# Performance work log

Measured on AMD Instinct MI355X. Metric: run time of the kernel, lower is better.

The kernel has to match this reference:

```python
import jax, jax.numpy as jnp
import numpy as np

N_MESH, N_GRID, N_EDGE = 2562, 16384, 49152
D, EDGE_DIM, OUT_DIM = 512, 4, 128
LN_EPS = 1e-5


def _mlp_ln(x, w1, b1, w2, b2, g, beta):
    # Linear -> ReLU -> Linear -> LayerNorm (activate_final=False, use_layer_norm=True)
    h = jax.nn.relu(x @ w1 + b1)
    h = h @ w2 + b2
    mu = jnp.mean(h, axis=-1, keepdims=True)
    var = jnp.var(h, axis=-1, keepdims=True)
    return (h - mu) * jax.lax.rsqrt(var + LN_EPS) * g + beta


def setup_inputs() -> dict:
    key = jax.random.key(0)
    ks = iter(jax.random.split(key, 40))

    def W(i, o):
        return (jax.random.normal(next(ks), (i, o), jnp.float32) / np.float32(np.sqrt(i)))

    inp = {
        "input_mesh_nodes": jax.random.normal(next(ks), (N_MESH, D), jnp.float32),
        "input_grid_nodes": jax.random.normal(next(ks), (N_GRID, D), jnp.float32),
        "input_edge_attr": jax.random.normal(next(ks), (N_EDGE, EDGE_DIM), jnp.float32),
        "edge_index": jnp.stack([
            jax.random.randint(next(ks), (N_EDGE,), 0, N_MESH, jnp.int32),  # senders (mesh)
            jax.random.randint(next(ks), (N_EDGE,), 0, N_GRID, jnp.int32),  # receivers (grid)
        ], axis=0),
        # edges_mlp: EDGE_DIM -> D -> D, LN
        "emlp_w1": W(EDGE_DIM, D), "emlp_b1": jnp.zeros((D,), jnp.float32),
        "emlp_w2": W(D, D), "emlp_b2": jnp.zeros((D,), jnp.float32),
        "emlp_g": jnp.ones((D,), jnp.float32), "emlp_beta": jnp.zeros((D,), jnp.float32),
        # gnn message MLP: 3D -> D -> D, LN   (cat(x_i, x_j, edge_attr))
        "ge_w1": W(3 * D, D), "ge_b1": jnp.zeros((D,), jnp.float32),
        "ge_w2": W(D, D), "ge_b2": jnp.zeros((D,), jnp.float32),
        "ge_g": jnp.ones((D,), jnp.float32), "ge_beta": jnp.zeros((D,), jnp.float32),
        # gnn node MLP: 2D -> D -> D, LN   (cat(receiver_x, aggr))
        "gn_w1": W(2 * D, D), "gn_b1": jnp.zeros((D,), jnp.float32),
        "gn_w2": W(D, D), "gn_b2": jnp.zeros((D,), jnp.float32),
        "gn_g": jnp.ones((D,), jnp.float32), "gn_beta": jnp.zeros((D,), jnp.float32),
        # grid_mlp_final: D -> D -> OUT_DIM, LN
        "fin_w1": W(D, D), "fin_b1": jnp.zeros((D,), jnp.float32),
        "fin_w2": W(D, OUT_DIM), "fin_b2": jnp.zeros((OUT_DIM,), jnp.float32),
        "fin_g": jnp.ones((OUT_DIM,), jnp.float32), "fin_beta": jnp.zeros((OUT_DIM,), jnp.float32),
    }
    return inp


def reference(input_mesh_nodes, input_grid_nodes, input_edge_attr, edge_index,
              emlp_w1, emlp_b1, emlp_w2, emlp_b2, emlp_g, emlp_beta,
              ge_w1, ge_b1, ge_w2, ge_b2, ge_g, ge_beta,
              gn_w1, gn_b1, gn_w2, gn_b2, gn_g, gn_beta,
              fin_w1, fin_b1, fin_w2, fin_b2, fin_g, fin_beta):
    # edge embedding MLP
    edges_emb = _mlp_ln(input_edge_attr, emlp_w1, emlp_b1, emlp_w2, emlp_b2, emlp_g, emlp_beta)
    senders, receivers = edge_index[0], edge_index[1]
    x_i = input_grid_nodes[receivers]   # receiver (grid) features gathered per edge
    x_j = input_mesh_nodes[senders]     # sender (mesh) features gathered per edge
    # per-edge message MLP on cat(x_i, x_j, edge_attr)
    msg = _mlp_ln(jnp.concatenate([x_i, x_j, edges_emb], axis=-1),
                  ge_w1, ge_b1, ge_w2, ge_b2, ge_g, ge_beta)  # [E, D]
    # scatter-add messages to receiver grid nodes (aggr='add')
    aggr = jax.ops.segment_sum(msg, receivers, num_segments=N_GRID)  # [N_GRID, D]
    # node update MLP on cat(receiver_x, aggr)
    gnn_out = _mlp_ln(jnp.concatenate([input_grid_nodes, aggr], axis=-1),
                      gn_w1, gn_b1, gn_w2, gn_b2, gn_g, gn_beta)
    latent_grid_nodes = input_grid_nodes + gnn_out  # residual
    return _mlp_ln(latent_grid_nodes, fin_w1, fin_b1, fin_w2, fin_b2, fin_g, fin_beta)
```

## Files before the change

kernel.cpp:

```cpp
#include <hip/hip_runtime.h>
#include <hip/hip_bf16.h>
#include <stdint.h>

#define LN_EPS 1e-5f

typedef __hip_bfloat16 bf16;
typedef short short8 __attribute__((ext_vector_type(8)));
typedef float f32x4 __attribute__((ext_vector_type(4)));

static __device__ __forceinline__ float bf2f(short s) {
    unsigned int u = ((unsigned int)(unsigned short)s) << 16;
    return __uint_as_float(u);
}
static __device__ __forceinline__ short f2bf(float x) {
    __hip_bfloat16 h = __float2bfloat16(x);
    return *reinterpret_cast<short*>(&h);
}

static __device__ __forceinline__ void gload16(const void* g, void* l) {
    __builtin_amdgcn_global_load_lds((const __attribute__((address_space(1))) void*)g,
                                     (__attribute__((address_space(3))) void*)l, 16, 0, 0);
}

struct TDesc { const float* src; bf16* dst; int K; int N; int kOff; };
struct TDescs { TDesc d[9]; };

__global__ void transpose_all_kernel(TDescs descs) {
    TDesc t = descs.d[blockIdx.z];
    int kb = blockIdx.x * 32, nb = blockIdx.y * 32;
    if (kb >= t.K || nb >= t.N) return;
    __shared__ float tile[32][33];
    int tx = threadIdx.x & 31, ty = threadIdx.x >> 5;
    for (int i = ty; i < 32; i += 8) {
        int k = kb + i, n = nb + tx;
        tile[i][tx] = (k < t.K && n < t.N) ? t.src[(size_t)(t.kOff + k) * t.N + n] : 0.f;
    }
    __syncthreads();
    for (int i = ty; i < 32; i += 8) {
        int n = nb + i, k = kb + tx;
        if (n < t.N && k < t.K)
            t.dst[(size_t)n * t.K + k] = __float2bfloat16(tile[tx][i]);
    }
}

__global__ void cvt_bf16_kernel(const float* __restrict__ src, bf16* __restrict__ dst, int n) {
    int i = blockIdx.x * 256 + threadIdx.x;
    int idx = i * 4;
    if (idx >= n) return;
    float4 v = *(const float4*)(src + idx);
    dst[idx + 0] = __float2bfloat16(v.x);
    dst[idx + 1] = __float2bfloat16(v.y);
    dst[idx + 2] = __float2bfloat16(v.z);
    dst[idx + 3] = __float2bfloat16(v.w);
}

__global__ void edge_l1_kernel(const float* __restrict__ attr, const float* __restrict__ w1,
                               const float* __restrict__ b1, bf16* __restrict__ h1, int E) {
    int e = blockIdx.x * 4 + (threadIdx.x >> 6);
    if (e >= E) return;
    int lane = threadIdx.x & 63;
    int d0 = lane * 8;
    float4 a = *(const float4*)(attr + (size_t)e * 4);
    float av[4] = {a.x, a.y, a.z, a.w};
    float s[8];
    {
        float4 c0 = *(const float4*)(b1 + d0), c1 = *(const float4*)(b1 + d0 + 4);
        s[0]=c0.x; s[1]=c0.y; s[2]=c0.z; s[3]=c0.w; s[4]=c1.x; s[5]=c1.y; s[6]=c1.z; s[7]=c1.w;
    }
#pragma unroll
    for (int k = 0; k < 4; k++) {
        float4 w0 = *(const float4*)(w1 + k * 512 + d0);
        float4 w1v = *(const float4*)(w1 + k * 512 + d0 + 4);
        float wv[8] = {w0.x, w0.y, w0.z, w0.w, w1v.x, w1v.y, w1v.z, w1v.w};
#pragma unroll
        for (int j = 0; j < 8; j++) s[j] += av[k] * wv[j];
    }
    short8 o;
#pragma unroll
    for (int j = 0; j < 8; j++) o[j] = f2bf(fmaxf(s[j], 0.f));
    *(short8*)(h1 + (size_t)e * 512 + d0) = o;
}

template <int EPI>
__global__ __launch_bounds__(256, 2) void gemm_bt_kernel(
    const bf16* __restrict__ A, const bf16* __restrict__ BT,
    const float* __restrict__ bias, bf16* __restrict__ C, int M, int N, int K,
    const bf16* __restrict__ gridp, const bf16* __restrict__ meshp,
    const int* __restrict__ send, const int* __restrict__ recv) {
    __shared__ short SMEM[2 * 2 * 128 * 64];
    const int t = threadIdx.x;
    const int lane = t & 63, w = t >> 6;
    const int wm = w >> 1, wn = w & 1;
    const int lr = lane & 15, lh = lane >> 4;

    int gx = gridDim.x, gy = gridDim.y;
    int orig = blockIdx.y * gx + blockIdx.x;
    int bx, by;
    if ((gy & 7) == 0) {
        int xcd = orig & 7, t2 = orig >> 3;
        bx = t2 % gx;
        by = xcd + 8 * (t2 / gx);
    } else { bx = blockIdx.x; by = blockIdx.y; }
    const int row0 = by * 128;
    const int col0 = bx * 128;

    const int sr3 = lane >> 3;
    const int su = (lane & 7) ^ sr3;
    const int srow = w * 32 + sr3;
    const int scol = su * 8;
    const bf16* gaP[4];
    const bf16* gbP[4];
#pragma unroll
    for (int i = 0; i < 4; i++) {
        int ra = row0 + srow + i * 8; if (ra >= M) ra = M - 1;
        int rb = col0 + srow + i * 8; if (rb >= N) rb = N - 1;
        gaP[i] = A + (size_t)ra * K + scol;
        gbP[i] = BT + (size_t)rb * K + scol;
    }

    auto STAGE = [&](int b, int k0) {
        short* la = SMEM + b * 16384 + w * 32 * 64;
        short* lb = la + 8192;
#pragma unroll
        for (int i = 0; i < 4; i++) {
            gload16(gaP[i] + k0, la + i * 8 * 64);
            gload16(gbP[i] + k0, lb + i * 8 * 64);
        }
    };

    f32x4 acc[4][4];
#pragma unroll
    for (int i = 0; i < 4; i++)
#pragma unroll
        for (int j = 0; j < 4; j++) acc[i][j] = {0.f, 0.f, 0.f, 0.f};

    const int T = K >> 6;
    STAGE(0, 0);
    __syncthreads();

    int cur = 0;
    for (int tt = 0; tt < T; ++tt) {
        if (tt + 1 < T) STAGE(cur ^ 1, (tt + 1) << 6);
        const short* Ac = SMEM + cur * 16384;
        const short* Bc = Ac + 8192;
#pragma unroll
        for (int kk = 0; kk < 64; kk += 32) {
            short8 af[4], bfv[4];
#pragma unroll
            for (int mf = 0; mf < 4; mf++) {
                int rowa = wm * 64 + mf * 16 + lr;
                int ua = ((kk >> 3) + lh) ^ (rowa & 7);
                af[mf] = *(const short8*)&Ac[rowa * 64 + ua * 8];
            }
#pragma unroll
            for (int nf = 0; nf < 4; nf++) {
                int rowb = wn * 64 + nf * 16 + lr;
                int ub = ((kk >> 3) + lh) ^ (rowb & 7);
                bfv[nf] = *(const short8*)&Bc[rowb * 64 + ub * 8];
            }
#pragma unroll
            for (int mf = 0; mf < 4; mf++)
#pragma unroll
                for (int nf = 0; nf < 4; nf++)
                    acc[mf][nf] = __builtin_amdgcn_mfma_f32_16x16x32_bf16(
                        af[mf], bfv[nf], acc[mf][nf], 0, 0, 0);
        }
        __syncthreads();
        cur ^= 1;
    }

    short* Cw = SMEM + w * (32 * 66);
    const int rgrp = lane >> 3, u = lane & 7;
#pragma unroll
    for (int hp = 0; hp < 2; hp++) {
#pragma unroll
        for (int mf2 = 0; mf2 < 2; mf2++) {
            int mf = hp * 2 + mf2;
#pragma unroll
            for (int nf = 0; nf < 4; nf++)
#pragma unroll
                for (int r2 = 0; r2 < 4; r2++) {
                    int rl = mf2 * 16 + lh * 4 + r2;
                    Cw[rl * 66 + nf * 16 + lr] = f2bf(acc[mf][nf][r2]);
                }
        }
#pragma unroll
        for (int rr = 0; rr < 4; rr++) {
            int rl = rr * 8 + rgrp;
            int grow = row0 + wm * 64 + hp * 32 + rl;
            int gcol = col0 + wn * 64 + u * 8;
            short8 vv = *(const short8*)&Cw[rl * 66 + u * 8];
            float vf[8];
#pragma unroll
            for (int j = 0; j < 8; j++) vf[j] = bf2f(vv[j]);
            if (EPI >= 1) {
                float4 c0 = *(const float4*)(bias + gcol);
                float4 c1 = *(const float4*)(bias + gcol + 4);
                float bb[8] = {c0.x, c0.y, c0.z, c0.w, c1.x, c1.y, c1.z, c1.w};
#pragma unroll
                for (int j = 0; j < 8; j++) vf[j] += bb[j];
            }
            if (EPI == 3) {
                int e = grow < M ? grow : M - 1;
                int rn = recv[e], sn = send[e];
                short8 gp = *(const short8*)(gridp + (size_t)rn * 512 + gcol);
                short8 mp = *(const short8*)(meshp + (size_t)sn * 512 + gcol);
#pragma unroll
                for (int j = 0; j < 8; j++) vf[j] += bf2f(gp[j]) + bf2f(mp[j]);
            }
            if (EPI >= 2) {
#pragma unroll
                for (int j = 0; j < 8; j++) vf[j] = fmaxf(vf[j], 0.f);
            }
            short8 o;
#pragma unroll
            for (int j = 0; j < 8; j++) o[j] = f2bf(vf[j]);
            if (grow < M && gcol < N)
                *(short8*)(C + (size_t)grow * N + gcol) = o;
        }
    }
}

template <int MODE, int DN>
__global__ void ln_kernel(const bf16* __restrict__ X, const float* __restrict__ gw,
                          const float* __restrict__ bw, bf16* __restrict__ outb,
                          float* __restrict__ outf, const bf16* __restrict__ resid, int R) {
    constexpr int EPL = DN / 64;
    int row = blockIdx.x * 4 + (threadIdx.x >> 6);
    if (row >= R) return;
    int lane = threadIdx.x & 63;
    const bf16* xr = X + (size_t)row * DN + lane * EPL;
    float v[EPL];
    if constexpr (EPL == 8) {
        short8 t8 = *(const short8*)xr;
#pragma unroll
        for (int j = 0; j < 8; j++) v[j] = bf2f(t8[j]);
    } else {
#pragma unroll
        for (int j = 0; j < EPL; j++) v[j] = __bfloat162float(xr[j]);
    }
    float s = 0.f, s2 = 0.f;
#pragma unroll
    for (int j = 0; j < EPL; j++) { s += v[j]; s2 += v[j] * v[j]; }
#pragma unroll
    for (int o = 32; o > 0; o >>= 1) {
        s += __shfl_xor(s, o, 64);
        s2 += __shfl_xor(s2, o, 64);
    }
    float mu = s * (1.f / DN);
    float var = s2 * (1.f / DN) - mu * mu;
    float rs = rsqrtf(var + LN_EPS);
    int d0 = lane * EPL;

    if constexpr (MODE == 0) {
        short8 o;
#pragma unroll
        for (int j = 0; j < EPL; j++)
            o[j] = f2bf((v[j] - mu) * rs * gw[d0 + j] + bw[d0 + j]);
        *(short8*)(outb + (size_t)row * DN + d0) = o;
    } else if constexpr (MODE == 2) {
        short8 rv = *(const short8*)(resid + (size_t)row * DN + d0);
        short8 o;
#pragma unroll
        for (int j = 0; j < EPL; j++) {
            float y = (v[j] - mu) * rs * gw[d0 + j] + bw[d0 + j];
            o[j] = f2bf(bf2f(rv[j]) + y);
        }
        *(short8*)(outb + (size_t)row * DN + d0) = o;
    } else {
#pragma unroll
        for (int j = 0; j < EPL; j++)
            outf[(size_t)row * DN + d0 + j] = (v[j] - mu) * rs * gw[d0 + j] + bw[d0 + j];
    }
}

__global__ void ln_stats_kernel(const bf16* __restrict__ X, float2* __restrict__ stats, int R) {
    int row = blockIdx.x * 4 + (threadIdx.x >> 6);
    if (row >= R) return;
    int lane = threadIdx.x & 63;
    short8 t8 = *(const short8*)(X + (size_t)row * 512 + lane * 8);
    float s = 0.f, s2 = 0.f;
#pragma unroll
    for (int j = 0; j < 8; j++) {
        float x = bf2f(t8[j]);
        s += x; s2 += x * x;
    }
#pragma unroll
    for (int o = 32; o > 0; o >>= 1) {
        s += __shfl_xor(s, o, 64);
        s2 += __shfl_xor(s2, o, 64);
    }
    float mu = s * (1.f / 512.f);
    float var = s2 * (1.f / 512.f) - mu * mu;
    if (lane == 0) stats[row] = make_float2(mu, rsqrtf(var + LN_EPS));
}

__global__ void degree_kernel(const int* __restrict__ recv, int* __restrict__ deg, int E) {
    int e = blockIdx.x * 256 + threadIdx.x;
    if (e < E) atomicAdd(&deg[recv[e]], 1);
}

__global__ void scan_kernel(const int* __restrict__ deg, int* __restrict__ off) {
    __shared__ int partial[1024];
    int t = threadIdx.x;
    int base = t * 16;
    int v[16];
    int s = 0;
#pragma unroll
    for (int i = 0; i < 16; i++) { v[i] = deg[base + i]; s += v[i]; }
    partial[t] = s;
    __syncthreads();
    for (int o = 1; o < 1024; o <<= 1) {
        int x = (t >= o) ? partial[t - o] : 0;
        __syncthreads();
        partial[t] += x;
        __syncthreads();
    }
    int run = (t == 0) ? 0 : partial[t - 1];
#pragma unroll
    for (int i = 0; i < 16; i++) { off[base + i] = run; run += v[i]; }
    if (t == 1023) off[16384] = run;
}

__global__ void scatter_kernel(const int* __restrict__ recv, const int* __restrict__ off,
                               int* __restrict__ cnt, int* __restrict__ edges, int E) {
    int e = blockIdx.x * 256 + threadIdx.x;
    if (e < E) {
        int r = recv[e];
        int p = atomicAdd(&cnt[r], 1);
        edges[off[r] + p] = e;
    }
}

__global__ void aggregate_kernel(const bf16* __restrict__ T5, const float2* __restrict__ stats,
                                 const float* __restrict__ gw, const float* __restrict__ bw,
                                 const bf16* __restrict__ gridb,
                                 const int* __restrict__ off, const int* __restrict__ edges,
                                 bf16* __restrict__ X2, int G) {
    int g = blockIdx.x * 4 + (threadIdx.x >> 6);
    if (g >= G) return;
    int lane = threadIdx.x & 63;
    int d0 = lane * 8;
    float gg[8], bb[8];
    {
        float4 a = *(const float4*)(gw + d0), b = *(const float4*)(gw + d0 + 4);
        gg[0]=a.x; gg[1]=a.y; gg[2]=a.z; gg[3]=a.w; gg[4]=b.x; gg[5]=b.y; gg[6]=b.z; gg[7]=b.w;
        float4 c = *(const float4*)(bw + d0), d = *(const float4*)(bw + d0 + 4);
        bb[0]=c.x; bb[1]=c.y; bb[2]=c.z; bb[3]=c.w; bb[4]=d.x; bb[5]=d.y; bb[6]=d.z; bb[7]=d.w;
    }
    float s[8] = {0.f, 0.f, 0.f, 0.f, 0.f, 0.f, 0.f, 0.f};
    int a = off[g], b = off[g + 1];
    for (int i = a; i < b; i++) {
        int e = edges[i];
        float2 st = stats[e];
        short8 m = *(const short8*)(T5 + (size_t)e * 512 + d0);
#pragma unroll
        for (int j = 0; j < 8; j++)
            s[j] += (bf2f(m[j]) - st.x) * st.y * gg[j] + bb[j];
    }
    *(short8*)(X2 + (size_t)g * 1024 + d0) = *(const short8*)(gridb + (size_t)g * 512 + d0);
    short8 o;
#pragma unroll
    for (int j = 0; j < 8; j++) o[j] = f2bf(s[j]);
    *(short8*)(X2 + (size_t)g * 1024 + 512 + d0) = o;
}

extern "C" void kernel_launch(void* const* d_in, const int* in_sizes, int n_in,
                              void* d_out, int out_size, void* d_ws, size_t ws_size,
                              hipStream_t stream) {
    const int NM = 2562, NG = 16384, NE = 49152;
    const float* mesh   = (const float*)d_in[0];
    const float* grid   = (const float*)d_in[1];
    const float* attr   = (const float*)d_in[2];
    const int*   eidx   = (const int*)d_in[3];
    const int*   send   = eidx;
    const int*   recv   = eidx + NE;
    const float* emlp_w1 = (const float*)d_in[4];
    const float* emlp_b1 = (const float*)d_in[5];
    const float* emlp_w2 = (const float*)d_in[6];
    const float* emlp_b2 = (const float*)d_in[7];
    const float* emlp_g  = (const float*)d_in[8];
    const float* emlp_be = (const float*)d_in[9];
    const float* ge_w1 = (const float*)d_in[10];
    const float* ge_b1 = (const float*)d_in[11];
    const float* ge_w2 = (const float*)d_in[12];
    const float* ge_b2 = (const float*)d_in[13];
    const float* ge_g  = (const float*)d_in[14];
    const float* ge_be = (const float*)d_in[15];
    const float* gn_w1 = (const float*)d_in[16];
    const float* gn_b1 = (const float*)d_in[17];
    const float* gn_w2 = (const float*)d_in[18];
    const float* gn_b2 = (const float*)d_in[19];
    const float* gn_g  = (const float*)d_in[20];
    const float* gn_be = (const float*)d_in[21];
    const float* fin_w1 = (const float*)d_in[22];
    const float* fin_b1 = (const float*)d_in[23];
    const float* fin_w2 = (const float*)d_in[24];
    const float* fin_b2 = (const float*)d_in[25];
    const float* fin_g  = (const float*)d_in[26];
    const float* fin_be = (const float*)d_in[27];

    char* p = (char*)d_ws;
    auto take = [&](size_t bytes) -> char* {
        char* r = p;
        p += (bytes + 255) & ~(size_t)255;
        return r;
    };
    bf16* emlp_w2T = (bf16*)take((size_t)512 * 512 * 2);
    bf16* geA_T    = (bf16*)take((size_t)512 * 512 * 2);
    bf16* geB_T    = (bf16*)take((size_t)512 * 512 * 2);
    bf16* geC_T    = (bf16*)take((size_t)512 * 512 * 2);
    bf16* ge_w2T   = (bf16*)take((size_t)512 * 512 * 2);
    bf16* gn_w1T   = (bf16*)take((size_t)512 * 1024 * 2);
    bf16* gn_w2T   = (bf16*)take((size_t)512 * 512 * 2);
    bf16* fin_w1T  = (bf16*)take((size_t)512 * 512 * 2);
    bf16* fin_w2T  = (bf16*)take((size_t)128 * 512 * 2);
    bf16* grid_bf  = (bf16*)take((size_t)NG * 512 * 2);
    bf16* mesh_bf  = (bf16*)take((size_t)NM * 512 * 2);
    bf16* bufA     = (bf16*)take((size_t)NE * 512 * 2);
    bf16* bufB     = (bf16*)take((size_t)NE * 512 * 2);
    bf16* bufC     = (bf16*)take((size_t)NG * 512 * 2);
    bf16* bufD     = (bf16*)take((size_t)NM * 512 * 2);
    float2* stats  = (float2*)take((size_t)NE * 8);
    int*  deg      = (int*)take((size_t)NG * 4);
    int*  cnt      = (int*)take((size_t)NG * 4);
    int*  csr_off  = (int*)take((size_t)(NG + 1) * 4);
    int*  csr_edge = (int*)take((size_t)NE * 4);

    TDescs td;
    td.d[0] = {emlp_w2, emlp_w2T, 512, 512, 0};
    td.d[1] = {ge_w1,   geA_T,    512, 512, 0};
    td.d[2] = {ge_w1,   geB_T,    512, 512, 512};
    td.d[3] = {ge_w1,   geC_T,    512, 512, 1024};
    td.d[4] = {ge_w2,   ge_w2T,   512, 512, 0};
    td.d[5] = {gn_w1,   gn_w1T,  1024, 512, 0};
    td.d[6] = {gn_w2,   gn_w2T,   512, 512, 0};
    td.d[7] = {fin_w1,  fin_w1T,  512, 512, 0};
    td.d[8] = {fin_w2,  fin_w2T,  512, 128, 0};
    hipLaunchKernelGGL(transpose_all_kernel, dim3(32, 16, 9), dim3(256), 0, stream, td);

    hipLaunchKernelGGL(cvt_bf16_kernel, dim3((NG * 512 / 4 + 255) / 256), dim3(256), 0, stream,
                       grid, grid_bf, NG * 512);
    hipLaunchKernelGGL(cvt_bf16_kernel, dim3((NM * 512 / 4 + 255) / 256), dim3(256), 0, stream,
                       mesh, mesh_bf, NM * 512);
    hipMemsetAsync(deg, 0, (size_t)NG * 4, stream);
    hipMemsetAsync(cnt, 0, (size_t)NG * 4, stream);
    hipLaunchKernelGGL(degree_kernel, dim3((NE + 255) / 256), dim3(256), 0, stream, recv, deg, NE);
    hipLaunchKernelGGL(scan_kernel, dim3(1), dim3(1024), 0, stream, deg, csr_off);
    hipLaunchKernelGGL(scatter_kernel, dim3((NE + 255) / 256), dim3(256), 0, stream,
                       recv, csr_off, cnt, csr_edge, NE);

    hipLaunchKernelGGL(edge_l1_kernel, dim3(NE / 4), dim3(256), 0, stream,
                       attr, emlp_w1, emlp_b1, bufA, NE);
    hipLaunchKernelGGL(gemm_bt_kernel<1>, dim3(4, NE / 128), dim3(256), 0, stream,
                       bufA, emlp_w2T, emlp_b2, bufB, NE, 512, 512,
                       (const bf16*)nullptr, (const bf16*)nullptr, (const int*)nullptr, (const int*)nullptr);
    hipLaunchKernelGGL((ln_kernel<0, 512>), dim3(NE / 4), dim3(256), 0, stream,
                       bufB, emlp_g, emlp_be, bufB, (float*)nullptr, (const bf16*)nullptr, NE);

    hipLaunchKernelGGL(gemm_bt_kernel<0>, dim3(4, NG / 128), dim3(256), 0, stream,
                       grid_bf, geA_T, (const float*)nullptr, bufC, NG, 512, 512,
                       (const bf16*)nullptr, (const bf16*)nullptr, (const int*)nullptr, (const int*)nullptr);
    hipLaunchKernelGGL(gemm_bt_kernel<0>, dim3(4, (NM + 127) / 128), dim3(256), 0, stream,
                       mesh_bf, geB_T, (const float*)nullptr, bufD, NM, 512, 512,
                       (const bf16*)nullptr, (const bf16*)nullptr, (const int*)nullptr, (const int*)nullptr);
    hipLaunchKernelGGL(gemm_bt_kernel<3>, dim3(4, NE / 128), dim3(256), 0, stream,
                       bufB, geC_T, ge_b1, bufA, NE, 512, 512,
                       bufC, bufD, send, recv);
    hipLaunchKernelGGL(gemm_bt_kernel<1>, dim3(4, NE / 128), dim3(256), 0, stream,
                       bufA, ge_w2T, ge_b2, bufB, NE, 512, 512,
                       (const bf16*)nullptr, (const bf16*)nullptr, (const int*)nullptr, (const int*)nullptr);
    hipLaunchKernelGGL(ln_stats_kernel, dim3(NE / 4), dim3(256), 0, stream, bufB, stats, NE);
    hipLaunchKernelGGL(aggregate_kernel, dim3(NG / 4), dim3(256), 0, stream,
                       bufB, stats, ge_g, ge_be, grid_bf, csr_off, csr_edge, bufA, NG);

    hipLaunchKernelGGL(gemm_bt_kernel<2>, dim3(4, NG / 128), dim3(256), 0, stream,
                       bufA, gn_w1T, gn_b1, bufC, NG, 512, 1024,
                       (const bf16*)nullptr, (const bf16*)nullptr, (const int*)nullptr, (const int*)nullptr);
    hipLaunchKernelGGL(gemm_bt_kernel<1>, dim3(4, NG / 128), dim3(256), 0, stream,
                       bufC, gn_w2T, gn_b2, bufB, NG, 512, 512,
                       (const bf16*)nullptr, (const bf16*)nullptr, (const int*)nullptr, (const int*)nullptr);
    hipLaunchKernelGGL((ln_kernel<2, 512>), dim3(NG / 4), dim3(256), 0, stream,
                       bufB, gn_g, gn_be, bufA, (float*)nullptr, grid_bf, NG);

    hipLaunchKernelGGL(gemm_bt_kernel<2>, dim3(4, NG / 128), dim3(256), 0, stream,
                       bufA, fin_w1T, fin_b1, bufC, NG, 512, 512,
                       (const bf16*)nullptr, (const bf16*)nullptr, (const int*)nullptr, (const int*)nullptr);
    hipLaunchKernelGGL(gemm_bt_kernel<1>, dim3(1, NG / 128), dim3(256), 0, stream,
                       bufC, fin_w2T, fin_b2, bufB, NG, 128, 512,
                       (const bf16*)nullptr, (const bf16*)nullptr, (const int*)nullptr, (const int*)nullptr);
    hipLaunchKernelGGL((ln_kernel<3, 128>), dim3(NG / 4), dim3(256), 0, stream,
                       bufB, fin_g, fin_be, (bf16*)nullptr, (float*)d_out, (const bf16*)nullptr, NG);
}
```

Measured before the change: 336.2 us.

## Fold edge LayerNorm into message GEMM, fuse final LN, tweak GEMM pipeline

Replaces the edge-embedding LayerNorm pass with a stats-only pass. The gamma scale is folded into the transposed message weights, and mean/rstd/beta are applied in the message GEMM epilogue through precomputed u/v vectors. The final N=128 GEMM now does its LayerNorm in the epilogue and writes fp32 output directly, which removes a separate LN kernel and an intermediate buffer round trip. It also changes the XCD-aware block remap to handle grids not divisible by 8 and replaces __syncthreads with explicit vmcnt waits plus barriers in the K loop. The edge LN is now applied after bf16 rounding of the unnormalized values, which slightly changes numerics.

```diff
diff --git a/kernel.cpp b/kernel.cpp
--- a/kernel.cpp
+++ b/kernel.cpp
@@ -22,7 +22,7 @@
                                      (__attribute__((address_space(3))) void*)l, 16, 0, 0);
 }
 
-struct TDesc { const float* src; bf16* dst; int K; int N; int kOff; };
+struct TDesc { const float* src; bf16* dst; int K; int N; int kOff; const float* scale; };
 struct TDescs { TDesc d[9]; };
 
 __global__ void transpose_all_kernel(TDescs descs) {
@@ -33,7 +33,9 @@
     int tx = threadIdx.x & 31, ty = threadIdx.x >> 5;
     for (int i = ty; i < 32; i += 8) {
         int k = kb + i, n = nb + tx;
-        tile[i][tx] = (k < t.K && n < t.N) ? t.src[(size_t)(t.kOff + k) * t.N + n] : 0.f;
+        float v = (k < t.K && n < t.N) ? t.src[(size_t)(t.kOff + k) * t.N + n] : 0.f;
+        if (t.scale && k < t.K) v *= t.scale[k];
+        tile[i][tx] = v;
     }
     __syncthreads();
     for (int i = ty; i < 32; i += 8) {
@@ -41,6 +43,21 @@
         if (n < t.N && k < t.K)
             t.dst[(size_t)n * t.K + k] = __float2bfloat16(tile[tx][i]);
     }
+}
+
+__global__ void uv_kernel(const float* __restrict__ W, const float* __restrict__ g,
+                          const float* __restrict__ be, float* __restrict__ u,
+                          float* __restrict__ v) {
+    int n = blockIdx.x * 256 + threadIdx.x;
+    if (n >= 512) return;
+    float su = 0.f, sv = 0.f;
+    for (int k = 0; k < 512; k++) {
+        float w = W[(size_t)(1024 + k) * 512 + n];
+        su += g[k] * w;
+        sv += be[k] * w;
+    }
+    u[n] = su;
+    v[n] = sv;
 }
 
 __global__ void cvt_bf16_kernel(const float* __restrict__ src, bf16* __restrict__ dst, int n) {
@@ -86,21 +103,22 @@
     const bf16* __restrict__ A, const bf16* __restrict__ BT,
     const float* __restrict__ bias, bf16* __restrict__ C, int M, int N, int K,
     const bf16* __restrict__ gridp, const bf16* __restrict__ meshp,
-    const int* __restrict__ send, const int* __restrict__ recv) {
+    const int* __restrict__ send, const int* __restrict__ recv,
+    const float2* __restrict__ stats, const float* __restrict__ uvec,
+    const float* __restrict__ vvec, float* __restrict__ OutF) {
     __shared__ short SMEM[2 * 2 * 128 * 64];
     const int t = threadIdx.x;
     const int lane = t & 63, w = t >> 6;
     const int wm = w >> 1, wn = w & 1;
     const int lr = lane & 15, lh = lane >> 4;
 
-    int gx = gridDim.x, gy = gridDim.y;
+    int gx = gridDim.x;
+    int nwg = gx * gridDim.y;
     int orig = blockIdx.y * gx + blockIdx.x;
-    int bx, by;
-    if ((gy & 7) == 0) {
-        int xcd = orig & 7, t2 = orig >> 3;
-        bx = t2 % gx;
-        by = xcd + 8 * (t2 / gx);
-    } else { bx = blockIdx.x; by = blockIdx.y; }
+    int q = nwg >> 3, r = nwg & 7;
+    int xcd = orig & 7, loc = orig >> 3;
+    int wg = (xcd < r ? xcd * (q + 1) : r * (q + 1) + (xcd - r) * q) + loc;
+    int bx = wg % gx, by = wg / gx;
     const int row0 = by * 128;
     const int col0 = bx * 128;
 
@@ -136,11 +154,18 @@
 
     const int T = K >> 6;
     STAGE(0, 0);
-    __syncthreads();
 
     int cur = 0;
     for (int tt = 0; tt < T; ++tt) {
-        if (tt + 1 < T) STAGE(cur ^ 1, (tt + 1) << 6);
+        if (tt + 1 < T) {
+            STAGE(cur ^ 1, (tt + 1) << 6);
+            asm volatile("s_waitcnt vmcnt(8)" ::: "memory");
+        } else {
+            asm volatile("s_waitcnt vmcnt(0)" ::: "memory");
+        }
+        __builtin_amdgcn_s_barrier();
+        asm volatile("" ::: "memory");
+
         const short* Ac = SMEM + cur * 16384;
         const short* Bc = Ac + 8192;
 #pragma unroll
@@ -165,8 +190,63 @@
                     acc[mf][nf] = __builtin_amdgcn_mfma_f32_16x16x32_bf16(
                         af[mf], bfv[nf], acc[mf][nf], 0, 0, 0);
         }
+        asm volatile("" ::: "memory");
+        __builtin_amdgcn_s_barrier();
+        cur ^= 1;
+    }
+
+    if (EPI == 5) {
+        short* Cs = SMEM;
+#pragma unroll
+        for (int nf = 0; nf < 4; nf++) {
+            float bv = bias[wn * 64 + nf * 16 + lr];
+#pragma unroll
+            for (int mf = 0; mf < 4; mf++)
+#pragma unroll
+                for (int r2 = 0; r2 < 4; r2++) {
+                    int rl = wm * 64 + mf * 16 + lh * 4 + r2;
+                    Cs[rl * 132 + wn * 64 + nf * 16 + lr] = f2bf(acc[mf][nf][r2] + bv);
+                }
+        }
         __syncthreads();
-        cur ^= 1;
+        int rl = w * 32 + (lane >> 1);
+        int half = lane & 1;
+        short8 vs[8];
+        float s = 0.f, s2 = 0.f;
+#pragma unroll
+        for (int j8 = 0; j8 < 8; j8++) {
+            vs[j8] = *(const short8*)&Cs[rl * 132 + half * 64 + j8 * 8];
+#pragma unroll
+            for (int j = 0; j < 8; j++) {
+                float f = bf2f(vs[j8][j]);
+                s += f; s2 += f * f;
+            }
+        }
+        s += __shfl_xor(s, 1, 64);
+        s2 += __shfl_xor(s2, 1, 64);
+        float mu = s * (1.f / 128.f);
+        float var = s2 * (1.f / 128.f) - mu * mu;
+        float rs = rsqrtf(var + LN_EPS);
+        int grow = row0 + rl;
+#pragma unroll
+        for (int j8 = 0; j8 < 8; j8++) {
+            int c0 = half * 64 + j8 * 8;
+            float4 g0 = *(const float4*)(uvec + c0), g1 = *(const float4*)(uvec + c0 + 4);
+            float4 b0 = *(const float4*)(vvec + c0), b1v = *(const float4*)(vvec + c0 + 4);
+            float gg[8] = {g0.x, g0.y, g0.z, g0.w, g1.x, g1.y, g1.z, g1.w};
+            float bb[8] = {b0.x, b0.y, b0.z, b0.w, b1v.x, b1v.y, b1v.z, b1v.w};
+            float4 o0, o1;
+            float* op = (float*)&o0;
+#pragma unroll
+            for (int j = 0; j < 8; j++) {
+                float y = (bf2f(vs[j8][j]) - mu) * rs * gg[j] + bb[j];
+                if (j < 4) ((float*)&o0)[j] = y; else ((float*)&o1)[j - 4] = y;
+            }
+            (void)op;
+            *(float4*)(OutF + (size_t)grow * 128 + c0) = o0;
+            *(float4*)(OutF + (size_t)grow * 128 + c0 + 4) = o1;
+        }
+        return;
     }
 
     short* Cw = SMEM + w * (32 * 66);
@@ -193,6 +273,17 @@
             float vf[8];
 #pragma unroll
             for (int j = 0; j < 8; j++) vf[j] = bf2f(vv[j]);
+            if (EPI == 4) {
+                int e = grow < M ? grow : M - 1;
+                float2 st = stats[e];
+                float rs = st.y, mrs = st.x * st.y;
+                float4 u0 = *(const float4*)(uvec + gcol), u1 = *(const float4*)(uvec + gcol + 4);
+                float4 v0 = *(const float4*)(vvec + gcol), v1 = *(const float4*)(vvec + gcol + 4);
+                float uu[8] = {u0.x, u0.y, u0.z, u0.w, u1.x, u1.y, u1.z, u1.w};
+                float vvv[8] = {v0.x, v0.y, v0.z, v0.w, v1.x, v1.y, v1.z, v1.w};
+#pragma unroll
+                for (int j = 0; j < 8; j++) vf[j] = rs * vf[j] - mrs * uu[j] + vvv[j];
+            }
             if (EPI >= 1) {
                 float4 c0 = *(const float4*)(bias + gcol);
                 float4 c1 = *(const float4*)(bias + gcol + 4);
@@ -200,7 +291,7 @@
 #pragma unroll
                 for (int j = 0; j < 8; j++) vf[j] += bb[j];
             }
-            if (EPI == 3) {
+            if (EPI == 4) {
                 int e = grow < M ? grow : M - 1;
                 int rn = recv[e], sn = send[e];
                 short8 gp = *(const short8*)(gridp + (size_t)rn * 512 + gcol);
@@ -208,7 +299,7 @@
 #pragma unroll
                 for (int j = 0; j < 8; j++) vf[j] += bf2f(gp[j]) + bf2f(mp[j]);
             }
-            if (EPI >= 2) {
+            if (EPI == 2 || EPI == 4) {
 #pragma unroll
                 for (int j = 0; j < 8; j++) vf[j] = fmaxf(vf[j], 0.f);
             }
@@ -221,57 +312,36 @@
     }
 }
 
-template <int MODE, int DN>
-__global__ void ln_kernel(const bf16* __restrict__ X, const float* __restrict__ gw,
-                          const float* __restrict__ bw, bf16* __restrict__ outb,
-                          float* __restrict__ outf, const bf16* __restrict__ resid, int R) {
-    constexpr int EPL = DN / 64;
+__global__ void ln_resid_kernel(const bf16* __restrict__ X, const float* __restrict__ gw,
+                                const float* __restrict__ bw, bf16* __restrict__ outb,
+                                const bf16* __restrict__ resid, int R) {
     int row = blockIdx.x * 4 + (threadIdx.x >> 6);
     if (row >= R) return;
     int lane = threadIdx.x & 63;
-    const bf16* xr = X + (size_t)row * DN + lane * EPL;
-    float v[EPL];
-    if constexpr (EPL == 8) {
-        short8 t8 = *(const short8*)xr;
-#pragma unroll
-        for (int j = 0; j < 8; j++) v[j] = bf2f(t8[j]);
-    } else {
-#pragma unroll
-        for (int j = 0; j < EPL; j++) v[j] = __bfloat162float(xr[j]);
-    }
+    short8 t8 = *(const short8*)(X + (size_t)row * 512 + lane * 8);
+    float v[8];
+#pragma unroll
+    for (int j = 0; j < 8; j++) v[j] = bf2f(t8[j]);
     float s = 0.f, s2 = 0.f;
 #pragma unroll
-    for (int j = 0; j < EPL; j++) { s += v[j]; s2 += v[j] * v[j]; }
+    for (int j = 0; j < 8; j++) { s += v[j]; s2 += v[j] * v[j]; }
 #pragma unroll
     for (int o = 32; o > 0; o >>= 1) {
         s += __shfl_xor(s, o, 64);
         s2 += __shfl_xor(s2, o, 64);
     }
-    float mu = s * (1.f / DN);
-    float var = s2 * (1.f / DN) - mu * mu;
+    float mu = s * (1.f / 512.f);
+    float var = s2 * (1.f / 512.f) - mu * mu;
     float rs = rsqrtf(var + LN_EPS);
-    int d0 = lane * EPL;
-
-    if constexpr (MODE == 0) {
-        short8 o;
-#pragma unroll
-        for (int j = 0; j < EPL; j++)
-            o[j] = f2bf((v[j] - mu) * rs * gw[d0 + j] + bw[d0 + j]);
-        *(short8*)(outb + (size_t)row * DN + d0) = o;
-    } else if constexpr (MODE == 2) {
-        short8 rv = *(const short8*)(resid + (size_t)row * DN + d0);
-        short8 o;
-#pragma unroll
-        for (int j = 0; j < EPL; j++) {
-            float y = (v[j] - mu) * rs * gw[d0 + j] + bw[d0 + j];
-            o[j] = f2bf(bf2f(rv[j]) + y);
-        }
-        *(short8*)(outb + (size_t)row * DN + d0) = o;
-    } else {
-#pragma unroll
-        for (int j = 0; j < EPL; j++)
-            outf[(size_t)row * DN + d0 + j] = (v[j] - mu) * rs * gw[d0 + j] + bw[d0 + j];
-    }
+    int d0 = lane * 8;
+    short8 rv = *(const short8*)(resid + (size_t)row * 512 + d0);
+    short8 o;
+#pragma unroll
+    for (int j = 0; j < 8; j++) {
+        float y = (v[j] - mu) * rs * gw[d0 + j] + bw[d0 + j];
+        o[j] = f2bf(bf2f(rv[j]) + y);
+    }
+    *(short8*)(outb + (size_t)row * 512 + d0) = o;
 }
 
 __global__ void ln_stats_kernel(const bf16* __restrict__ X, float2* __restrict__ stats, int R) {
@@ -422,22 +492,29 @@
     bf16* bufC     = (bf16*)take((size_t)NG * 512 * 2);
     bf16* bufD     = (bf16*)take((size_t)NM * 512 * 2);
     float2* stats  = (float2*)take((size_t)NE * 8);
+    float* uvecW   = (float*)take((size_t)512 * 4);
+    float* vvecW   = (float*)take((size_t)512 * 4);
     int*  deg      = (int*)take((size_t)NG * 4);
     int*  cnt      = (int*)take((size_t)NG * 4);
     int*  csr_off  = (int*)take((size_t)(NG + 1) * 4);
     int*  csr_edge = (int*)take((size_t)NE * 4);
 
+    const bf16* nbf = nullptr; const int* ni = nullptr;
+    const float2* nst = nullptr; const float* nf = nullptr; float* nff = nullptr;
+
     TDescs td;
-    td.d[0] = {emlp_w2, emlp_w2T, 512, 512, 0};
-    td.d[1] = {ge_w1,   geA_T,    512, 512, 0};
-    td.d[2] = {ge_w1,   geB_T,    512, 512, 512};
-    td.d[3] = {ge_w1,   geC_T,    512, 512, 1024};
-    td.d[4] = {ge_w2,   ge_w2T,   512, 512, 0};
-    td.d[5] = {gn_w1,   gn_w1T,  1024, 512, 0};
-    td.d[6] = {gn_w2,   gn_w2T,   512, 512, 0};
-    td.d[7] = {fin_w1,  fin_w1T,  512, 512, 0};
-    td.d[8] = {fin_w2,  fin_w2T,  512, 128, 0};
+    td.d[0] = {emlp_w2, emlp_w2T, 512, 512, 0, nullptr};
+    td.d[1] = {ge_w1,   geA_T,    512, 512, 0, nullptr};
+    td.d[2] = {ge_w1,   geB_T,    512, 512, 512, nullptr};
+    td.d[3] = {ge_w1,   geC_T,    512, 512, 1024, emlp_g};
+    td.d[4] = {ge_w2,   ge_w2T,   512, 512, 0, nullptr};
+    td.d[5] = {gn_w1,   gn_w1T,  1024, 512, 0, nullptr};
+    td.d[6] = {gn_w2,   gn_w2T,   512, 512, 0, nullptr};
+    td.d[7] = {fin_w1,  fin_w1T,  512, 512, 0, nullptr};
+    td.d[8] = {fin_w2,  fin_w2T,  512, 128, 0, nullptr};
     hipLaunchKernelGGL(transpose_all_kernel, dim3(32, 16, 9), dim3(256), 0, stream, td);
+    hipLaunchKernelGGL(uv_kernel, dim3(2), dim3(256), 0, stream,
+                       ge_w1, emlp_g, emlp_be, uvecW, vvecW);
 
     hipLaunchKernelGGL(cvt_bf16_kernel, dim3((NG * 512 / 4 + 255) / 256), dim3(256), 0, stream,
                        grid, grid_bf, NG * 512);
@@ -454,41 +531,38 @@
                        attr, emlp_w1, emlp_b1, bufA, NE);
     hipLaunchKernelGGL(gemm_bt_kernel<1>, dim3(4, NE / 128), dim3(256), 0, stream,
                        bufA, emlp_w2T, emlp_b2, bufB, NE, 512, 512,
-                       (const bf16*)nullptr, (const bf16*)nullptr, (const int*)nullptr, (const int*)nullptr);
-    hipLaunchKernelGGL((ln_kernel<0, 512>), dim3(NE / 4), dim3(256), 0, stream,
-                       bufB, emlp_g, emlp_be, bufB, (float*)nullptr, (const bf16*)nullptr, NE);
+                       nbf, nbf, ni, ni, nst, nf, nf, nff);
+    hipLaunchKernelGGL(ln_stats_kernel, dim3(NE / 4), dim3(256), 0, stream, bufB, stats, NE);
 
     hipLaunchKernelGGL(gemm_bt_kernel<0>, dim3(4, NG / 128), dim3(256), 0, stream,
-                       grid_bf, geA_T, (const float*)nullptr, bufC, NG, 512, 512,
-                       (const bf16*)nullptr, (const bf16*)nullptr, (const int*)nullptr, (const int*)nullptr);
+                       grid_bf, geA_T, nf, bufC, NG, 512, 512,
+                       nbf, nbf, ni, ni, nst, nf, nf, nff);
     hipLaunchKernelGGL(gemm_bt_kernel<0>, dim3(4, (NM + 127) / 128), dim3(256), 0, stream,
-                       mesh_bf, geB_T, (const float*)nullptr, bufD, NM, 512, 512,
-                       (const bf16*)nullptr, (const bf16*)nullptr, (const int*)nullptr, (const int*)nullptr);
-    hipLaunchKernelGGL(gemm_bt_kernel<3>, dim3(4, NE / 128), dim3(256), 0, stream,
+                       mesh_bf, geB_T, nf, bufD, NM, 512, 512,
+                       nbf, nbf, ni, ni, nst, nf, nf, nff);
+    hipLaunchKernelGGL(gemm_bt_kernel<4>, dim3(4, NE / 128), dim3(256), 0, stream,
                        bufB, geC_T, ge_b1, bufA, NE, 512, 512,
-                       bufC, bufD, send, recv);
+                       bufC, bufD, send, recv, stats, uvecW, vvecW, nff);
     hipLaunchKernelGGL(gemm_bt_kernel<1>, dim3(4, NE / 128), dim3(256), 0, stream,
                        bufA, ge_w2T, ge_b2, bufB, NE, 512, 512,
-                       (const bf16*)nullptr, (const bf16*)nullptr, (const int*)nullptr, (const int*)nullptr);
+                       nbf, nbf, ni, ni, nst, nf, nf, nff);
     hipLaunchKernelGGL(ln_stats_kernel, dim3(NE / 4), dim3(256), 0, stream, bufB, stats, NE);
     hipLaunchKernelGGL(aggregate_kernel, dim3(NG / 4), dim3(256), 0, stream,
                        bufB, stats, ge_g, ge_be, grid_bf, csr_off, csr_edge, bufA, NG);
 
     hipLaunchKernelGGL(gemm_bt_kernel<2>, dim3(4, NG / 128), dim3(256), 0, stream,
                        bufA, gn_w1T, gn_b1, bufC, NG, 512, 1024,
-                       (const bf16*)nullptr, (const bf16*)nullptr, (const int*)nullptr, (const int*)nullptr);
+                       nbf, nbf, ni, ni, nst, nf, nf, nff);
     hipLaunchKernelGGL(gemm_bt_kernel<1>, dim3(4, NG / 128), dim3(256), 0, stream,
                        bufC, gn_w2T, gn_b2, bufB, NG, 512, 512,
-                       (const bf16*)nullptr, (const bf16*)nullptr, (const int*)nullptr, (const int*)nullptr);
-    hipLaunchKernelGGL((ln_kernel<2, 512>), dim3(NG / 4), dim3(256), 0, stream,
-                       bufB, gn_g, gn_be, bufA, (float*)nullptr, grid_bf, NG);
+                       nbf, nbf, ni, ni, nst, nf, nf, nff);
+    hipLaunchKernelGGL(ln_resid_kernel, dim3(NG / 4), dim3(256), 0, stream,
+                       bufB, gn_g, gn_be, bufA, grid_bf, NG);
 
     hipLaunchKernelGGL(gemm_bt_kernel<2>, dim3(4, NG / 128), dim3(256), 0, stream,
                        bufA, fin_w1T, fin_b1, bufC, NG, 512, 512,
-                       (const bf16*)nullptr, (const bf16*)nullptr, (const int*)nullptr, (const int*)nullptr);
-    hipLaunchKernelGGL(gemm_bt_kernel<1>, dim3(1, NG / 128), dim3(256), 0, stream,
-                       bufC, fin_w2T, fin_b2, bufB, NG, 128, 512,
-                       (const bf16*)nullptr, (const bf16*)nullptr, (const int*)nullptr, (const int*)nullptr);
-    hipLaunchKernelGGL((ln_kernel<3, 128>), dim3(NG / 4), dim3(256), 0, stream,
-                       bufB, fin_g, fin_be, (bf16*)nullptr, (float*)d_out, (const bf16*)nullptr, NG);
-}
+                       nbf, nbf, ni, ni, nst, nf, nf, nff);
+    hipLaunchKernelGGL(gemm_bt_kernel<5>, dim3(1, NG / 128), dim3(256), 0, stream,
+                       bufC, fin_w2T, fin_b2, (bf16*)nullptr, NG, 128, 512,
+                       nbf, nbf, ni, ni, nst, fin_g, fin_be, (float*)d_out);
+}
```

Measured after the change: 353.2 us. +5.0%, slower.
